# Kernel optimization log

Measured on AMD Instinct MI355X. Metric: run time of the kernel, lower is better.

## Reference

```python
import jax, jax.numpy as jnp
import numpy as np
from jax import lax

NUM_CLASSES = 19
BINS_NUM = 51
LOSS_WEIGHT = 1.0


def setup_inputs() -> dict:
    key = jax.random.key(0)
    k1, k2 = jax.random.split(key)
    feature = jax.random.normal(k1, (1, 256, 64, 64), dtype=jnp.float32)
    label = jax.random.randint(k2, (1, 1, 64, 64), 0, NUM_CLASSES).astype(jnp.int64)
    return {"feature": feature, "label": label}


def reference(feature, label):
    # feature: [1, D, H, W]; label: [1, 1, H, W] (same spatial size -> nearest resize is identity)
    D = feature.shape[1]
    C = NUM_CLASSES
    F = feature[0].reshape(D, -1).T            # [N, D] pixel feature vectors
    L = label[0, 0].reshape(-1).astype(jnp.int32)  # [N] class id per pixel

    counts = jax.ops.segment_sum(jnp.ones(L.shape, jnp.float32), L, num_segments=C)  # [C]
    sum_f = jax.ops.segment_sum(F, L, num_segments=C)        # [C, D]
    sum_f2 = jax.ops.segment_sum(F * F, L, num_segments=C)   # [C, D]
    has = counts > 0
    cnt = jnp.maximum(counts, 1.0)
    miu = sum_f / cnt[:, None]                                # first-iter: direct assignment (no EMA yet)
    moment2 = sum_f2 / cnt[:, None]
    var = jnp.maximum(moment2 - miu ** 2, 1e-12)
    # stats are computed via detached numpy in the original -> no grad
    miu = lax.stop_gradient(miu)
    var = lax.stop_gradient(var)
    var_sample = var / 25.0

    bins = jnp.linspace(-5.0, 5.0, BINS_NUM).astype(jnp.float32)  # [B]

    # target gaussian pdf per (class, feature-dim, bin): [C, D, B]
    inv_norm_t = 1.0 / jnp.sqrt(2.0 * jnp.pi * var)
    target = jnp.exp(-0.5 * (bins[None, None, :] - miu[:, :, None]) ** 2 / var[:, :, None]) * inv_norm_t[:, :, None]

    # sample KDE per pixel, scatter-added into its class: [N, D, B] -> [C, D, B]
    vs_p = var_sample[L]                                      # [N, D]
    inv_norm_s = 1.0 / jnp.sqrt(2.0 * jnp.pi * vs_p)          # [N, D]
    K = jnp.exp(-0.5 * (bins[None, None, :] - F[:, :, None]) ** 2 / vs_p[:, :, None]) * inv_norm_s[:, :, None]
    samp = jax.ops.segment_sum(K, L, num_segments=C)          # [C, D, B]

    samp_den = jnp.where(has[:, None], jnp.maximum(samp.sum(-1), 1e-30), 1.0)[:, :, None]
    tgt_den = jnp.where(has[:, None], jnp.maximum(target.sum(-1), 1e-30), 1.0)[:, :, None]
    hist = samp / samp_den
    target = target / tgt_den

    # smooth L1 (beta=1, mean reduction) per class
    diff = hist - target
    ad = jnp.abs(diff)
    sl1 = jnp.where(ad < 1.0, 0.5 * diff * diff, ad - 0.5).mean(axis=(1, 2))  # [C]

    active = has & (jnp.arange(C) > 0)
    active_num = jnp.sum(active.astype(jnp.float32))
    loss = jnp.sum(jnp.where(active, sl1, 0.0)) / (active_num + 1e-12)
    return (LOSS_WEIGHT * loss, feature)
```

## Files before the change

kernel.cpp:

```cpp
#include <hip/hip_runtime.h>

#define N_PIX 4096
#define N_D   256
#define N_C   19
#define N_B   51

#define OFF_LIST   0
#define OFF_COUNTS 311296
#define OFF_ACC    311424

__global__ __launch_bounds__(256) void k_bucket(const int* __restrict__ label,
                                                int* __restrict__ list,
                                                int* __restrict__ counts,
                                                float* __restrict__ acc) {
    const int c = blockIdx.x;
    const int w = threadIdx.x >> 6;
    const int lane = threadIdx.x & 63;
    __shared__ int wcnt[4];
    if (c == 0 && threadIdx.x == 0) *acc = 0.f;

    const int q0 = w * 1024;
    int cnt = 0;
    for (int base = 0; base < 1024; base += 64) {
        const bool match = (label[q0 + base + lane] == c);
        cnt += (int)__popcll(__ballot(match));
    }
    if (lane == 0) wcnt[w] = cnt;
    __syncthreads();
    int m = 0;
#pragma unroll
    for (int i = 0; i < 4; ++i) m += (i < w) ? wcnt[i] : 0;

    for (int base = 0; base < 1024; base += 64) {
        const int n = q0 + base + lane;
        const bool match = (label[n] == c);
        const unsigned long long mask = __ballot(match);
        if (match) list[c * N_PIX + m + __popcll(mask & ((1ull << lane) - 1ull))] = n;
        m += (int)__popcll(mask);
    }
    if (w == 3 && lane == 0) counts[c] = m;
}

__global__ __launch_bounds__(256) void k_main(const float* __restrict__ feature,
                                              const int* __restrict__ list,
                                              const int* __restrict__ counts,
                                              float* __restrict__ acc) {
    const int c = blockIdx.x + 1;
    const int w = threadIdx.x >> 6;
    const int d = blockIdx.y * 4 + w;
    const int lane = threadIdx.x & 63;
    const int m = counts[c];
    __shared__ float blk[4];
    float part = 0.f;
    if (m > 0) {
        const float* __restrict__ row = feature + d * N_PIX;
        const int* __restrict__ lst = list + c * N_PIX;

        float s1 = 0.f, s2 = 0.f;
        for (int j = lane; j < m; j += 64) {
            const float f = row[lst[j]];
            s1 += f;
            s2 += f * f;
        }
#pragma unroll
        for (int off = 32; off; off >>= 1) {
            s1 += __shfl_xor(s1, off);
            s2 += __shfl_xor(s2, off);
        }
        const float cnt = (float)m;
        const float mu = s1 / cnt;
        const float v = fmaxf(s2 / cnt - mu * mu, 1e-12f);

        const float LOG2E = 1.44269504088896340736f;
        const float as = -12.5f * LOG2E / v;
        const float at = -0.5f * LOG2E / v;
        const float bin = (lane < N_B) ? fmaf(0.2f, (float)lane, -5.0f) : 1e18f;
        const float tt = bin - mu;
        const float targ = __builtin_amdgcn_exp2f(at * tt * tt);

        float acc_s = 0.f;
        for (int base = 0; base < m; base += 64) {
            const int j = base + lane;
            const float fl = (j < m) ? row[lst[j]] : -1e18f;
#pragma unroll
            for (int k = 0; k < 64; ++k) {
                const float f = __shfl(fl, k);
                const float t = f - bin;
                acc_s += __builtin_amdgcn_exp2f(as * t * t);
            }
        }

        float ss = acc_s, st = targ;
#pragma unroll
        for (int off = 32; off; off >>= 1) {
            ss += __shfl_xor(ss, off);
            st += __shfl_xor(st, off);
        }
        const float hist = acc_s / fmaxf(ss, 1e-30f);
        const float tgt  = targ  / fmaxf(st, 1e-30f);
        const float diff = hist - tgt;
        const float ad = fabsf(diff);
        float sl1 = (ad < 1.f) ? 0.5f * diff * diff : ad - 0.5f;
#pragma unroll
        for (int off = 32; off; off >>= 1) sl1 += __shfl_down(sl1, off);
        part = sl1;
    }
    if (lane == 0) blk[w] = part;
    __syncthreads();
    if (threadIdx.x == 0) atomicAdd(acc, blk[0] + blk[1] + blk[2] + blk[3]);
}

__global__ __launch_bounds__(64) void k_final(const int* __restrict__ counts,
                                              const float* __restrict__ acc,
                                              float* __restrict__ out) {
    if (threadIdx.x == 0) {
        int active = 0;
        for (int c = 1; c < N_C; ++c) active += (counts[c] > 0) ? 1 : 0;
        out[0] = (*acc) / (float)(N_D * N_B) / ((float)active + 1e-12f);
    }
}

extern "C" void kernel_launch(void* const* d_in, const int* in_sizes, int n_in,
                              void* d_out, int out_size, void* d_ws, size_t ws_size,
                              hipStream_t stream) {
    const float* feature = (const float*)d_in[0];
    const int* label = (const int*)d_in[1];
    float* out = (float*)d_out;
    char* ws = (char*)d_ws;
    int* list = (int*)(ws + OFF_LIST);
    int* counts = (int*)(ws + OFF_COUNTS);
    float* acc = (float*)(ws + OFF_ACC);

    hipMemcpyAsync(out + 1, feature, (size_t)N_PIX * N_D * sizeof(float),
                   hipMemcpyDeviceToDevice, stream);

    k_bucket<<<N_C, 256, 0, stream>>>(label, list, counts, acc);
    dim3 grid(N_C - 1, N_D / 4);
    k_main<<<grid, 256, 0, stream>>>(feature, list, counts, acc);
    k_final<<<1, 64, 0, stream>>>(counts, acc, out);
}
```

Before: 97.18 us.

## Fuse feature copy into bucketing kernel and finalize via last-block ticket

Replaces the separate device-to-device memcpy with extra blocks of the bucketing kernel that copy the feature tensor with float4 loads and scalar stores, since the output starts at offset 1 and is misaligned. Removes the final single-thread kernel by having the last k_main block, found through an atomic ticket counter, compute the loss. Splits the KDE inner loop into four independent accumulators to break the serial add dependence chain. This cuts launch overhead and the separate copy, at the cost of unaligned scalar stores and dependence on atomic ordering.

```diff
diff --git a/kernel.cpp b/kernel.cpp
--- a/kernel.cpp
+++ b/kernel.cpp
@@ -4,47 +4,68 @@
 #define N_D   256
 #define N_C   19
 #define N_B   51
+#define N_BLOCKS_MAIN (18 * 64)
 
 #define OFF_LIST   0
 #define OFF_COUNTS 311296
 #define OFF_ACC    311424
+#define OFF_TICKET 311428
 
-__global__ __launch_bounds__(256) void k_bucket(const int* __restrict__ label,
-                                                int* __restrict__ list,
-                                                int* __restrict__ counts,
-                                                float* __restrict__ acc) {
-    const int c = blockIdx.x;
-    const int w = threadIdx.x >> 6;
-    const int lane = threadIdx.x & 63;
-    __shared__ int wcnt[4];
-    if (c == 0 && threadIdx.x == 0) *acc = 0.f;
+__global__ __launch_bounds__(256) void k_pre(const float* __restrict__ feature,
+                                             const int* __restrict__ label,
+                                             float* __restrict__ out,
+                                             int* __restrict__ list,
+                                             int* __restrict__ counts,
+                                             float* __restrict__ acc,
+                                             int* __restrict__ ticket) {
+    const int b = blockIdx.x;
+    if (b < N_C) {
+        const int c = b;
+        const int w = threadIdx.x >> 6;
+        const int lane = threadIdx.x & 63;
+        __shared__ int wcnt[4];
+        if (c == 0 && threadIdx.x == 0) { *acc = 0.f; *ticket = 0; }
 
-    const int q0 = w * 1024;
-    int cnt = 0;
-    for (int base = 0; base < 1024; base += 64) {
-        const bool match = (label[q0 + base + lane] == c);
-        cnt += (int)__popcll(__ballot(match));
+        const int q0 = w * 1024;
+        int cnt = 0;
+        for (int base = 0; base < 1024; base += 64) {
+            cnt += (int)__popcll(__ballot(label[q0 + base + lane] == c));
+        }
+        if (lane == 0) wcnt[w] = cnt;
+        __syncthreads();
+        int m = 0;
+#pragma unroll
+        for (int i = 0; i < 4; ++i) m += (i < w) ? wcnt[i] : 0;
+
+        for (int base = 0; base < 1024; base += 64) {
+            const int n = q0 + base + lane;
+            const bool match = (label[n] == c);
+            const unsigned long long mask = __ballot(match);
+            if (match) list[c * N_PIX + m + __popcll(mask & ((1ull << lane) - 1ull))] = n;
+            m += (int)__popcll(mask);
+        }
+        if (w == 3 && lane == 0) counts[c] = m;
+    } else {
+        const int tid = (b - N_C) * 256 + threadIdx.x;
+        const int nth = (256 - N_C) * 256;
+        const float4* __restrict__ src = (const float4*)feature;
+        float* __restrict__ dst = out + 1;
+        for (int i = tid; i < N_PIX * N_D / 4; i += nth) {
+            const float4 v = src[i];
+            dst[4 * i + 0] = v.x;
+            dst[4 * i + 1] = v.y;
+            dst[4 * i + 2] = v.z;
+            dst[4 * i + 3] = v.w;
+        }
     }
-    if (lane == 0) wcnt[w] = cnt;
-    __syncthreads();
-    int m = 0;
-#pragma unroll
-    for (int i = 0; i < 4; ++i) m += (i < w) ? wcnt[i] : 0;
-
-    for (int base = 0; base < 1024; base += 64) {
-        const int n = q0 + base + lane;
-        const bool match = (label[n] == c);
-        const unsigned long long mask = __ballot(match);
-        if (match) list[c * N_PIX + m + __popcll(mask & ((1ull << lane) - 1ull))] = n;
-        m += (int)__popcll(mask);
-    }
-    if (w == 3 && lane == 0) counts[c] = m;
 }
 
 __global__ __launch_bounds__(256) void k_main(const float* __restrict__ feature,
                                               const int* __restrict__ list,
                                               const int* __restrict__ counts,
-                                              float* __restrict__ acc) {
+                                              float* __restrict__ acc,
+                                              int* __restrict__ ticket,
+                                              float* __restrict__ out) {
     const int c = blockIdx.x + 1;
     const int w = threadIdx.x >> 6;
     const int d = blockIdx.y * 4 + w;
@@ -78,17 +99,24 @@
         const float tt = bin - mu;
         const float targ = __builtin_amdgcn_exp2f(at * tt * tt);
 
-        float acc_s = 0.f;
+        float a0 = 0.f, a1 = 0.f, a2 = 0.f, a3 = 0.f;
         for (int base = 0; base < m; base += 64) {
             const int j = base + lane;
             const float fl = (j < m) ? row[lst[j]] : -1e18f;
 #pragma unroll
-            for (int k = 0; k < 64; ++k) {
-                const float f = __shfl(fl, k);
-                const float t = f - bin;
-                acc_s += __builtin_amdgcn_exp2f(as * t * t);
+            for (int k = 0; k < 64; k += 4) {
+                const float f0 = __shfl(fl, k);
+                const float f1 = __shfl(fl, k + 1);
+                const float f2 = __shfl(fl, k + 2);
+                const float f3 = __shfl(fl, k + 3);
+                const float t0 = f0 - bin, t1 = f1 - bin, t2 = f2 - bin, t3 = f3 - bin;
+                a0 += __builtin_amdgcn_exp2f(as * t0 * t0);
+                a1 += __builtin_amdgcn_exp2f(as * t1 * t1);
+                a2 += __builtin_amdgcn_exp2f(as * t2 * t2);
+                a3 += __builtin_amdgcn_exp2f(as * t3 * t3);
             }
         }
+        const float acc_s = (a0 + a1) + (a2 + a3);
 
         float ss = acc_s, st = targ;
 #pragma unroll
@@ -107,16 +135,16 @@
     }
     if (lane == 0) blk[w] = part;
     __syncthreads();
-    if (threadIdx.x == 0) atomicAdd(acc, blk[0] + blk[1] + blk[2] + blk[3]);
-}
-
-__global__ __launch_bounds__(64) void k_final(const int* __restrict__ counts,
-                                              const float* __restrict__ acc,
-                                              float* __restrict__ out) {
     if (threadIdx.x == 0) {
-        int active = 0;
-        for (int c = 1; c < N_C; ++c) active += (counts[c] > 0) ? 1 : 0;
-        out[0] = (*acc) / (float)(N_D * N_B) / ((float)active + 1e-12f);
+        atomicAdd(acc, blk[0] + blk[1] + blk[2] + blk[3]);
+        __threadfence();
+        const int t = atomicAdd(ticket, 1);
+        if (t == N_BLOCKS_MAIN - 1) {
+            int active = 0;
+            for (int cc = 1; cc < N_C; ++cc) active += (counts[cc] > 0) ? 1 : 0;
+            const float total = atomicAdd(acc, 0.0f);
+            out[0] = total / (float)(N_D * N_B) / ((float)active + 1e-12f);
+        }
     }
 }
 
@@ -130,12 +158,9 @@
     int* list = (int*)(ws + OFF_LIST);
     int* counts = (int*)(ws + OFF_COUNTS);
     float* acc = (float*)(ws + OFF_ACC);
+    int* ticket = (int*)(ws + OFF_TICKET);
 
-    hipMemcpyAsync(out + 1, feature, (size_t)N_PIX * N_D * sizeof(float),
-                   hipMemcpyDeviceToDevice, stream);
-
-    k_bucket<<<N_C, 256, 0, stream>>>(label, list, counts, acc);
+    k_pre<<<256, 256, 0, stream>>>(feature, label, out, list, counts, acc, ticket);
     dim3 grid(N_C - 1, N_D / 4);
-    k_main<<<grid, 256, 0, stream>>>(feature, list, counts, acc);
-    k_final<<<1, 64, 0, stream>>>(counts, acc, out);
+    k_main<<<grid, 256, 0, stream>>>(feature, list, counts, acc, ticket, out);
 }
```

New measurement: 104.6 us. 7.6% more time.
